# Kernel optimization log

Hardware: AMD Instinct MI355X
Metric: run time of the kernel (lower is better)

Reference implementation:

```python
import jax, jax.numpy as jnp
import numpy as np

NUM_HEADS = 8

def _spline_scores(x):
    # x: (BH, S, E), softmax-normalized. Kernel per pair (i,j):
    #   sum_{e,f} [ max*min + 0.5*min^2*max - min^3/6 ] + E^2
    # using min*max = a*b  =>  a*b*(1 + 0.5*min) - min^3/6
    E = x.shape[-1]
    xi = x[:, :, None, :, None]          # (BH, S, 1, E, 1)
    xj = x[:, None, :, None, :]          # (BH, 1, S, 1, E)
    m = jnp.minimum(xi, xj)              # (BH, S, S, E, E)
    k = xi * xj * (1.0 + 0.5 * m) - (m * m * m) * (1.0 / 6.0)
    return k.sum(axis=(-1, -2)) + jnp.asarray(E * E, x.dtype)  # (BH, S, S)

def setup_inputs() -> dict:
    key = jax.random.key(0)
    k1, k2, k3 = jax.random.split(key, 3)
    B, S, D = 2, 128, 256
    scale = 1.0 / np.sqrt(D)
    return {
        "inputs": jax.random.normal(k1, (B, S, D), dtype=jnp.float32),
        "w_in": jax.random.normal(k2, (D, D), dtype=jnp.float32) * scale,
        "b_in": jnp.zeros((D,), dtype=jnp.float32),
        "w_out": jax.random.normal(k3, (D, D), dtype=jnp.float32) * scale,
        "b_out": jnp.zeros((D,), dtype=jnp.float32),
    }

def reference(inputs, w_in, b_in, w_out, b_out):
    B, S, D = inputs.shape
    H = NUM_HEADS
    E = D // H
    x = jnp.einsum('bsd,ed->bse', inputs, w_in) + b_in          # in_project (torch Linear: x @ W.T + b)
    x = x.reshape(B, S, H, E).transpose(0, 2, 1, 3).reshape(B * H, S, E)
    x = jax.nn.softmax(x, axis=-1)
    attn = _spline_scores(x) / E                                 # (BH, S, S)
    attn = jax.nn.softmax(attn, axis=-1)                         # dropout is identity at inference
    out = jnp.einsum('bij,bje->bie', attn, x)                    # (BH, S, E)
    out = out.reshape(B, H, S, E).transpose(0, 2, 1, 3).reshape(B, S, D)
    return jnp.einsum('bsd,ed->bse', out, w_out) + b_out
```

## Files before the change

### kernel.cpp

```cpp
#include <hip/hip_runtime.h>
#include <math.h>

constexpr int BB = 2;
constexpr int SS = 128;
constexpr int DD = 256;
constexpr int HH = 8;
constexpr int EE = 32;

__global__ __launch_bounds__(256) void spline_k1(
    const float* __restrict__ inp,
    const float* __restrict__ w_in,
    const float* __restrict__ b_in,
    float* __restrict__ xs_out)
{
  const int row = blockIdx.x;
  const int e = threadIdx.x;
  __shared__ float in_row[DD];
  __shared__ float vals[DD];
  __shared__ float exps[DD];

  in_row[e] = inp[row * DD + e];
  __syncthreads();

  const float* wr = w_in + e * DD;
  float acc = b_in[e];
#pragma unroll 8
  for (int d = 0; d < DD; d += 4) {
    const float4 w4 = *reinterpret_cast<const float4*>(wr + d);
    acc = fmaf(in_row[d + 0], w4.x, acc);
    acc = fmaf(in_row[d + 1], w4.y, acc);
    acc = fmaf(in_row[d + 2], w4.z, acc);
    acc = fmaf(in_row[d + 3], w4.w, acc);
  }
  vals[e] = acc;
  __syncthreads();

  const int h = e >> 5;
  const int base = h * EE;
  float mx = -1e30f;
#pragma unroll
  for (int k = 0; k < EE; ++k) mx = fmaxf(mx, vals[base + k]);
  const float ex = __expf(acc - mx);
  exps[e] = ex;
  __syncthreads();
  float sum = 0.f;
#pragma unroll
  for (int k = 0; k < EE; ++k) sum += exps[base + k];
  const float x = ex / sum;

  const int b = row / SS, s = row - b * SS;
  const int ee = e & 31;
  xs_out[(((b * HH + h) * SS) + s) * EE + ee] = x;
}

__global__ __launch_bounds__(128) void spline_k2a(
    const float* __restrict__ xs_g,
    float* __restrict__ sc_g)
{
  const int p = blockIdx.x;
  const int bh = blockIdx.y;
  const int t = threadIdx.x;

  __shared__ float xs[SS * EE];
  const float4* s4 = (const float4*)(xs_g + bh * SS * EE);
  float4* x4 = (float4*)xs;
#pragma unroll
  for (int k = 0; k < 8; ++k) x4[t + 128 * k] = s4[t + 128 * k];
  __syncthreads();

  int i, j;
  bool active = true;
  if (p == 0) { i = 0; j = t; }
  else if (p == 64) {
    if (t < 64) { i = 64; j = 64 + t; } else { i = 0; j = 0; active = false; }
  } else {
    if (t >= p) { i = p; j = t; }
    else        { i = 128 - p; j = 128 - p + t; }
  }

  float vrow[EE];
  float sv = 0.f;
#pragma unroll
  for (int k = 0; k < EE; ++k) {
    vrow[k] = xs[j * EE + ((k + t) & 31)];
    sv += vrow[k];
  }

  float a0 = 0.f, a1 = 0.f, a2 = 0.f, a3 = 0.f, su = 0.f;
  const int ibase = i * EE;
#pragma unroll 4
  for (int e1 = 0; e1 < EE; ++e1) {
    const float u = xs[ibase + e1];
    su += u;
#pragma unroll
    for (int e2 = 0; e2 < EE; e2 += 4) {
      { const float v = vrow[e2 + 0], m = fminf(u, v), pm = u * v, w = m * m;
        const float q2 = fmaf(w, -(1.f / 3.f), pm); a0 = fmaf(m, q2, a0); }
      { const float v = vrow[e2 + 1], m = fminf(u, v), pm = u * v, w = m * m;
        const float q2 = fmaf(w, -(1.f / 3.f), pm); a1 = fmaf(m, q2, a1); }
      { const float v = vrow[e2 + 2], m = fminf(u, v), pm = u * v, w = m * m;
        const float q2 = fmaf(w, -(1.f / 3.f), pm); a2 = fmaf(m, q2, a2); }
      { const float v = vrow[e2 + 3], m = fminf(u, v), pm = u * v, w = m * m;
        const float q2 = fmaf(w, -(1.f / 3.f), pm); a3 = fmaf(m, q2, a3); }
    }
  }
  const float mins = 0.5f * ((a0 + a1) + (a2 + a3));
  const float logit = (fmaf(su, sv, mins) + (float)(EE * EE)) * (1.0f / (float)EE);

  if (active) {
    float* base = sc_g + bh * SS * SS;
    base[i * SS + j] = logit;
    if (i != j) base[j * SS + i] = logit;
  }
}

__global__ __launch_bounds__(128) void spline_k2b(
    const float* __restrict__ sc_g,
    const float* __restrict__ xs_g,
    float* __restrict__ y)
{
  const int i = blockIdx.x;
  const int bh = blockIdx.y;
  const int t = threadIdx.x;

  __shared__ float xs[SS * EE];
  __shared__ float at[SS];
  __shared__ float part[128];
  __shared__ float wred[4];

  const float4* s4 = (const float4*)(xs_g + bh * SS * EE);
  float4* x4 = (float4*)xs;
#pragma unroll
  for (int k = 0; k < 8; ++k) x4[t + 128 * k] = s4[t + 128 * k];

  const float logit = sc_g[(bh * SS + i) * SS + t];

  float mx = logit;
#pragma unroll
  for (int off = 32; off; off >>= 1) mx = fmaxf(mx, __shfl_xor(mx, off));
  const int wid = t >> 6;
  if ((t & 63) == 0) wred[wid] = mx;
  __syncthreads();
  mx = fmaxf(wred[0], wred[1]);

  const float ex = __expf(logit - mx);
  float sm = ex;
#pragma unroll
  for (int off = 32; off; off >>= 1) sm += __shfl_xor(sm, off);
  __syncthreads();
  if ((t & 63) == 0) wred[2 + wid] = sm;
  at[t] = ex;
  __syncthreads();
  const float rs = 1.0f / (wred[2] + wred[3]);

  const int e = t & 31, q = t >> 5;
  float o = 0.f;
#pragma unroll
  for (int jj = 0; jj < 32; ++jj) {
    const int j = q * 32 + jj;
    o = fmaf(at[j], xs[j * EE + e], o);
  }
  part[t] = o;
  __syncthreads();
  if (t < 32) {
    const float oo = (part[t] + part[t + 32] + part[t + 64] + part[t + 96]) * rs;
    const int b = bh >> 3, h = bh & 7;
    y[(b * SS + i) * DD + h * EE + t] = oo;
  }
}

__global__ __launch_bounds__(256) void spline_k3(
    const float* __restrict__ y,
    const float* __restrict__ w_out,
    const float* __restrict__ b_out,
    float* __restrict__ out)
{
  const int row = blockIdx.x;
  const int e = threadIdx.x;
  __shared__ float yr[DD];
  yr[e] = y[row * DD + e];
  __syncthreads();

  const float* wr = w_out + e * DD;
  float acc = b_out[e];
#pragma unroll 8
  for (int d = 0; d < DD; d += 4) {
    const float4 w4 = *reinterpret_cast<const float4*>(wr + d);
    acc = fmaf(yr[d + 0], w4.x, acc);
    acc = fmaf(yr[d + 1], w4.y, acc);
    acc = fmaf(yr[d + 2], w4.z, acc);
    acc = fmaf(yr[d + 3], w4.w, acc);
  }
  out[row * DD + e] = acc;
}

extern "C" void kernel_launch(void* const* d_in, const int* in_sizes, int n_in,
                              void* d_out, int out_size, void* d_ws, size_t ws_size,
                              hipStream_t stream) {
  const float* inp   = (const float*)d_in[0];
  const float* w_in  = (const float*)d_in[1];
  const float* b_in  = (const float*)d_in[2];
  const float* w_out = (const float*)d_in[3];
  const float* b_out = (const float*)d_in[4];
  float* out = (float*)d_out;

  float* ws_x  = (float*)d_ws;
  float* ws_sc = ws_x + BB * HH * SS * EE;
  float* ws_y  = ws_sc + BB * HH * SS * SS;

  spline_k1<<<BB * SS, 256, 0, stream>>>(inp, w_in, b_in, ws_x);
  spline_k2a<<<dim3(65, BB * HH), 128, 0, stream>>>(ws_x, ws_sc);
  spline_k2b<<<dim3(SS, BB * HH), 128, 0, stream>>>(ws_sc, ws_x, ws_y);
  spline_k3<<<BB * SS, 256, 0, stream>>>(ws_y, w_out, b_out, out);
}
```

Baseline: 103.4 us.

## Replace pairwise E×E spline sum with sorted prefix-sum formulation fused into softmax

Kernel 1 now sorts each row's 32 softmax values with a warp bitonic sort and builds prefix sums of x, x², x³, packing them per row. The score kernel computes each pair's E×E min-based sum in O(E log E), using a binary search of each of j's values into i's sorted list plus closed-form sums, instead of the O(E²) loop. This removes the separate score kernel and its score-matrix round trip through global memory. The trade-off is divergent shared-memory binary searches and a different floating-point summation order.

```diff
diff --git a/kernel.cpp b/kernel.cpp
--- a/kernel.cpp
+++ b/kernel.cpp
@@ -6,12 +6,14 @@
 constexpr int DD = 256;
 constexpr int HH = 8;
 constexpr int EE = 32;
-
-__global__ __launch_bounds__(256) void spline_k1(
+constexpr int PKG = 132;
+
+__global__ __launch_bounds__(256) void spline_ka(
     const float* __restrict__ inp,
     const float* __restrict__ w_in,
     const float* __restrict__ b_in,
-    float* __restrict__ xs_out)
+    float* __restrict__ xs_out,
+    float* __restrict__ pkg_g)
 {
   const int row = blockIdx.x;
   const int e = threadIdx.x;
@@ -35,8 +37,7 @@
   vals[e] = acc;
   __syncthreads();
 
-  const int h = e >> 5;
-  const int base = h * EE;
+  const int h = e >> 5, base = h * EE, l = e & 31;
   float mx = -1e30f;
 #pragma unroll
   for (int k = 0; k < EE; ++k) mx = fmaxf(mx, vals[base + k]);
@@ -48,75 +49,40 @@
   for (int k = 0; k < EE; ++k) sum += exps[base + k];
   const float x = ex / sum;
 
-  const int b = row / SS, s = row - b * SS;
-  const int ee = e & 31;
-  xs_out[(((b * HH + h) * SS) + s) * EE + ee] = x;
-}
-
-__global__ __launch_bounds__(128) void spline_k2a(
+  const int b = row >> 7, s = row & 127;
+  const int bh = b * HH + h;
+  xs_out[(bh * SS + s) * EE + l] = x;
+
+  float v = x;
+#pragma unroll
+  for (int k = 2; k <= 32; k <<= 1) {
+#pragma unroll
+    for (int j = k >> 1; j > 0; j >>= 1) {
+      const float o = __shfl_xor(v, j, 32);
+      const bool up = ((l & k) == 0);
+      const bool tmin = (((l & j) == 0) == up);
+      v = tmin ? fminf(v, o) : fmaxf(v, o);
+    }
+  }
+  float i1 = v, i2 = v * v, i3 = v * v * v;
+#pragma unroll
+  for (int j = 1; j < 32; j <<= 1) {
+    const float o1 = __shfl_up(i1, j, 32);
+    const float o2 = __shfl_up(i2, j, 32);
+    const float o3 = __shfl_up(i3, j, 32);
+    if (l >= j) { i1 += o1; i2 += o2; i3 += o3; }
+  }
+  float* pk = pkg_g + (bh * SS + s) * PKG;
+  pk[l] = v;
+  pk[32 + l + 1] = i1;
+  pk[65 + l + 1] = i2;
+  pk[98 + l + 1] = i3;
+  if (l == 0) { pk[32] = 0.f; pk[65] = 0.f; pk[98] = 0.f; }
+}
+
+__global__ __launch_bounds__(128) void spline_kb(
     const float* __restrict__ xs_g,
-    float* __restrict__ sc_g)
-{
-  const int p = blockIdx.x;
-  const int bh = blockIdx.y;
-  const int t = threadIdx.x;
-
-  __shared__ float xs[SS * EE];
-  const float4* s4 = (const float4*)(xs_g + bh * SS * EE);
-  float4* x4 = (float4*)xs;
-#pragma unroll
-  for (int k = 0; k < 8; ++k) x4[t + 128 * k] = s4[t + 128 * k];
-  __syncthreads();
-
-  int i, j;
-  bool active = true;
-  if (p == 0) { i = 0; j = t; }
-  else if (p == 64) {
-    if (t < 64) { i = 64; j = 64 + t; } else { i = 0; j = 0; active = false; }
-  } else {
-    if (t >= p) { i = p; j = t; }
-    else        { i = 128 - p; j = 128 - p + t; }
-  }
-
-  float vrow[EE];
-  float sv = 0.f;
-#pragma unroll
-  for (int k = 0; k < EE; ++k) {
-    vrow[k] = xs[j * EE + ((k + t) & 31)];
-    sv += vrow[k];
-  }
-
-  float a0 = 0.f, a1 = 0.f, a2 = 0.f, a3 = 0.f, su = 0.f;
-  const int ibase = i * EE;
-#pragma unroll 4
-  for (int e1 = 0; e1 < EE; ++e1) {
-    const float u = xs[ibase + e1];
-    su += u;
-#pragma unroll
-    for (int e2 = 0; e2 < EE; e2 += 4) {
-      { const float v = vrow[e2 + 0], m = fminf(u, v), pm = u * v, w = m * m;
-        const float q2 = fmaf(w, -(1.f / 3.f), pm); a0 = fmaf(m, q2, a0); }
-      { const float v = vrow[e2 + 1], m = fminf(u, v), pm = u * v, w = m * m;
-        const float q2 = fmaf(w, -(1.f / 3.f), pm); a1 = fmaf(m, q2, a1); }
-      { const float v = vrow[e2 + 2], m = fminf(u, v), pm = u * v, w = m * m;
-        const float q2 = fmaf(w, -(1.f / 3.f), pm); a2 = fmaf(m, q2, a2); }
-      { const float v = vrow[e2 + 3], m = fminf(u, v), pm = u * v, w = m * m;
-        const float q2 = fmaf(w, -(1.f / 3.f), pm); a3 = fmaf(m, q2, a3); }
-    }
-  }
-  const float mins = 0.5f * ((a0 + a1) + (a2 + a3));
-  const float logit = (fmaf(su, sv, mins) + (float)(EE * EE)) * (1.0f / (float)EE);
-
-  if (active) {
-    float* base = sc_g + bh * SS * SS;
-    base[i * SS + j] = logit;
-    if (i != j) base[j * SS + i] = logit;
-  }
-}
-
-__global__ __launch_bounds__(128) void spline_k2b(
-    const float* __restrict__ sc_g,
-    const float* __restrict__ xs_g,
+    const float* __restrict__ pkg_g,
     float* __restrict__ y)
 {
   const int i = blockIdx.x;
@@ -124,6 +90,7 @@
   const int t = threadIdx.x;
 
   __shared__ float xs[SS * EE];
+  __shared__ float pkv[131];
   __shared__ float at[SS];
   __shared__ float part[128];
   __shared__ float wred[4];
@@ -132,8 +99,43 @@
   float4* x4 = (float4*)xs;
 #pragma unroll
   for (int k = 0; k < 8; ++k) x4[t + 128 * k] = s4[t + 128 * k];
-
-  const float logit = sc_g[(bh * SS + i) * SS + t];
+  const float* pk = pkg_g + (bh * SS + i) * PKG;
+  if (t < 131) pkv[t] = pk[t];
+  float vreg[EE];
+  {
+    const float4* vr4 = (const float4*)(xs_g + (bh * SS + t) * EE);
+    float4* vv = (float4*)vreg;
+#pragma unroll
+    for (int k = 0; k < 8; ++k) vv[k] = vr4[k];
+  }
+  __syncthreads();
+
+  const float* sI = pkv;
+  const float* P1 = pkv + 32;
+  const float* P2 = pkv + 65;
+  const float* P3 = pkv + 98;
+  const float T1 = P1[32];
+
+  float A = 0.f, B = 0.f, C = 0.f, Dg = 0.f, sv = 0.f;
+#pragma unroll
+  for (int bb = 0; bb < EE; ++bb) {
+    const float v = vreg[bb];
+    sv += v;
+    int idx = 0;
+#pragma unroll
+    for (int off = 16; off > 0; off >>= 1)
+      if (sI[idx + off - 1] <= v) idx += off;
+    if (sI[idx] <= v) ++idx;
+    const float g1 = P1[idx], g2 = P2[idx], g3 = P3[idx];
+    const float v2 = v * v;
+    const float fi = (float)idx - 32.0f;
+    A = fmaf(v, g2, A);
+    B = fmaf(v2, T1 - g1, B);
+    C = fmaf(v2 * v, fi, C);
+    Dg += g3;
+  }
+  const float sumF = fmaf(0.5f, A + B, (C - Dg) * (1.f / 6.f));
+  const float logit = (fmaf(T1, sv, sumF) + (float)(EE * EE)) * (1.0f / (float)EE);
 
   float mx = logit;
 #pragma unroll
@@ -162,7 +164,7 @@
   }
   part[t] = o;
   __syncthreads();
-  if (t < 32) {
+  if (t < EE) {
     const float oo = (part[t] + part[t + 32] + part[t + 64] + part[t + 96]) * rs;
     const int b = bh >> 3, h = bh & 7;
     y[(b * SS + i) * DD + h * EE + t] = oo;
@@ -204,12 +206,11 @@
   const float* b_out = (const float*)d_in[4];
   float* out = (float*)d_out;
 
-  float* ws_x  = (float*)d_ws;
-  float* ws_sc = ws_x + BB * HH * SS * EE;
-  float* ws_y  = ws_sc + BB * HH * SS * SS;
-
-  spline_k1<<<BB * SS, 256, 0, stream>>>(inp, w_in, b_in, ws_x);
-  spline_k2a<<<dim3(65, BB * HH), 128, 0, stream>>>(ws_x, ws_sc);
-  spline_k2b<<<dim3(SS, BB * HH), 128, 0, stream>>>(ws_sc, ws_x, ws_y);
+  float* ws_x   = (float*)d_ws;
+  float* ws_pkg = ws_x + BB * HH * SS * EE;
+  float* ws_y   = ws_pkg + BB * HH * SS * PKG;
+
+  spline_ka<<<BB * SS, 256, 0, stream>>>(inp, w_in, b_in, ws_x, ws_pkg);
+  spline_kb<<<dim3(SS, BB * HH), 128, 0, stream>>>(ws_x, ws_pkg, ws_y);
   spline_k3<<<BB * SS, 256, 0, stream>>>(ws_y, w_out, b_out, out);
 }
```

Result: faster. 91.88 us (-11.1%).
